# Kernel optimization log

Hardware: AMD Instinct MI355X
Metric: run time of the kernel (lower is better)

The kernel has to match this reference:

```python
import jax, jax.numpy as jnp
import numpy as np

N_HEAD = 16
N_EMBD = 1024
HEAD_DIM = N_EMBD // N_HEAD  # 64
ROPE_BASE = 10000.0


def _rotary_cos_sin(T, dim, dtype=jnp.float32):
    # matches Rotary: inv_freq over even indices, cos/sin cached in bfloat16
    inv_freq = 1.0 / (ROPE_BASE ** (jnp.arange(0, dim, 2, dtype=jnp.float32) / dim))
    freqs = jnp.arange(T, dtype=jnp.float32)[:, None] * inv_freq[None, :]  # [T, dim/2]
    cos = jnp.cos(freqs).astype(jnp.bfloat16).astype(dtype)
    sin = jnp.sin(freqs).astype(jnp.bfloat16).astype(dtype)
    # shape [1, T, 1, dim/2] to broadcast over (B, T, H, d)
    return cos[None, :, None, :], sin[None, :, None, :]


def _apply_rotary(x, cos, sin):
    d = x.shape[3] // 2
    x1, x2 = x[..., :d], x[..., d:]
    y1 = x1 * cos + x2 * sin
    y2 = -x1 * sin + x2 * cos
    return jnp.concatenate([y1, y2], axis=3).astype(x.dtype)


def setup_inputs() -> dict:
    key = jax.random.key(0)
    ks = jax.random.split(key, 8)
    B, T, C = 2, 2048, N_EMBD
    scale = C ** -0.5  # realistic linear-layer init scale
    x = jax.random.normal(ks[0], (B, T, C), dtype=jnp.float32)
    Wq1 = jax.random.normal(ks[1], (C, C), dtype=jnp.float32) * scale
    Wk1 = jax.random.normal(ks[2], (C, C), dtype=jnp.float32) * scale
    Wq2 = jax.random.normal(ks[3], (C, C), dtype=jnp.float32) * scale
    Wk2 = jax.random.normal(ks[4], (C, C), dtype=jnp.float32) * scale
    Wv = jax.random.normal(ks[5], (C, C), dtype=jnp.float32) * scale
    Wout = jax.random.normal(ks[6], (C, C), dtype=jnp.float32) * scale
    return {"x": x, "Wq1": Wq1, "Wk1": Wk1, "Wq2": Wq2, "Wk2": Wk2, "Wv": Wv, "Wout": Wout}


def reference(x, Wq1, Wk1, Wq2, Wk2, Wv, Wout):
    B, T, C = x.shape
    H, D = N_HEAD, HEAD_DIM

    def proj(W):
        # torch nn.Linear(bias=False): y = x @ W.T
        return (x @ W.T).reshape(B, T, H, D)

    q1, k1 = proj(Wq1), proj(Wk1)
    q2, k2 = proj(Wq2), proj(Wk2)
    v = proj(Wv)

    cos, sin = _rotary_cos_sin(T, D, x.dtype)
    q1, k1 = _apply_rotary(q1, cos, sin), _apply_rotary(k1, cos, sin)
    q2, k2 = _apply_rotary(q2, cos, sin), _apply_rotary(k2, cos, sin)

    # two bilinear score maps, elementwise product, causal mask
    s1 = jnp.einsum('bqhd,bkhd->bhqk', q1, k1)  # [B,H,T,T]
    s2 = jnp.einsum('bqhd,bkhd->bhqk', q2, k2)
    causal = jnp.tril(jnp.ones((T, T), dtype=bool))
    pattern = jnp.where(causal[None, None], (s1 / D) * (s2 / D), 0.0)

    y = jnp.einsum('bhqk,bkhd->bqhd', pattern, v).reshape(B, T, C)
    return y @ Wout.T
```

## Files before the change

kernel.cpp:

```cpp
#include <hip/hip_runtime.h>
#include <hip/hip_bf16.h>
#include <math.h>

typedef __bf16 bf16;
typedef __bf16 bf16x8 __attribute__((ext_vector_type(8)));
typedef float  f32x4  __attribute__((ext_vector_type(4)));

#define NB    2
#define NT    2048
#define NH    16
#define ND    64
#define NC    1024
#define NBT   4096
#define NQT   32

#define AS1C(p) ((const __attribute__((address_space(1))) void*)(p))
#define AS3(p)  ((__attribute__((address_space(3))) void*)(p))

#define MFMA(a,b,c) __builtin_amdgcn_mfma_f32_16x16x32_bf16(a, b, c, 0, 0, 0)

struct WPtrs { const float* p[6]; };

__global__ void prep_kernel(const float* __restrict__ x, WPtrs w,
                            bf16* __restrict__ Xbf, bf16* __restrict__ Wcat,
                            float2* __restrict__ tbl)
{
    const int bid = blockIdx.x;
    if (bid < 4096) {
        const int i = (bid * 256 + threadIdx.x) * 4;
        float4 v = *reinterpret_cast<const float4*>(x + i);
        Xbf[i+0] = (bf16)v.x; Xbf[i+1] = (bf16)v.y;
        Xbf[i+2] = (bf16)v.z; Xbf[i+3] = (bf16)v.w;
    } else if (bid < 10240) {
        const int r   = bid - 4096;
        const int mat = r >> 10;
        const int off = ((r & 1023) * 256 + threadIdx.x) * 4;
        float4 v = *reinterpret_cast<const float4*>(w.p[mat] + off);
        bf16* d = Wcat + (size_t)mat * NC * NC + off;
        d[0] = (bf16)v.x; d[1] = (bf16)v.y; d[2] = (bf16)v.z; d[3] = (bf16)v.w;
    } else {
        const int i = (bid - 10240) * 256 + threadIdx.x;
        const int t = i >> 5, j = i & 31;
        float invf = 1.0f / powf(10000.0f, (float)j * (1.0f/32.0f));
        float fr = (float)t * invf;
        float2 cs;
        cs.x = (float)(bf16)cosf(fr);
        cs.y = (float)(bf16)sinf(fr);
        tbl[i] = cs;
    }
}

__global__ __launch_bounds__(256, 3)
void gemm_proj(const bf16* __restrict__ A, const bf16* __restrict__ Bw,
               bf16* __restrict__ qkv, const float2* __restrict__ tbl)
{
    __shared__ bf16 smem[3*8192];

    const int tid  = threadIdx.x;
    const int lane = tid & 63;
    const int w    = tid >> 6;
    const int wr   = w >> 1;
    const int wc   = w & 1;

    const int id  = blockIdx.x;
    const int xcd = id & 7;
    const int r   = id >> 3;
    const int bx  = r >> 2;
    const int by  = xcd * 4 + (r & 3);
    const int row0 = by * 128, col0 = bx * 128;

    const int lo  = lane & 15;
    const int hi  = lane >> 4;

    const int hrow = w*16 + (lane >> 2);
    const int hcol = ((lane & 3) ^ ((lane >> 3) & 3)) * 8;

    f32x4 acc[4][4] = {};

    auto stageHalf = [&](int s, int slot) {
        char* base = (char*)smem + slot * 16384;
        const int k0 = s * 32;
        #pragma unroll
        for (int i = 0; i < 2; ++i) {
            __builtin_amdgcn_global_load_lds(
                AS1C(A + (size_t)(row0 + i*64 + hrow) * NC + k0 + hcol),
                AS3(base + i*4096 + w*1024), 16, 0, 0);
            __builtin_amdgcn_global_load_lds(
                AS1C(Bw + (size_t)(col0 + i*64 + hrow) * NC + k0 + hcol),
                AS3(base + 8192 + i*4096 + w*1024), 16, 0, 0);
        }
    };

    stageHalf(0, 0);
    stageHalf(1, 1);

    const int csw = (lo >> 1) & 3;
    int slot = 0;
    for (int s = 0; s < 32; ++s) {
        if (s < 31) asm volatile("s_waitcnt vmcnt(4)" ::: "memory");
        else        asm volatile("s_waitcnt vmcnt(0)" ::: "memory");
        __builtin_amdgcn_s_barrier();
        asm volatile("" ::: "memory");
        if (s + 2 < 32) {
            int nx = slot + 2; if (nx >= 3) nx -= 3;
            stageHalf(s + 2, nx);
        }

        const char* As = (const char*)smem + slot * 16384;
        const char* Bs = As + 8192;

        bf16x8 af[4], bfr[4];
        #pragma unroll
        for (int m = 0; m < 4; ++m) {
            const int ar = wr*64 + m*16 + lo;
            af[m] = *reinterpret_cast<const bf16x8*>(As + ar*64 + ((hi ^ csw) * 16));
        }
        #pragma unroll
        for (int n = 0; n < 4; ++n) {
            const int br = wc*64 + n*16 + lo;
            bfr[n] = *reinterpret_cast<const bf16x8*>(Bs + br*64 + ((hi ^ csw) * 16));
        }
        __builtin_amdgcn_s_setprio(1);
        #pragma unroll
        for (int m = 0; m < 4; ++m)
            #pragma unroll
            for (int n = 0; n < 4; ++n)
                acc[m][n] = MFMA(af[m], bfr[n], acc[m][n]);
        __builtin_amdgcn_s_setprio(0);

        slot += 1; if (slot >= 3) slot -= 3;
    }
    __syncthreads();

    bf16* Ct = smem;
    const int p  = col0 >> 10;
    const int h0 = (col0 >> 6) & (NH-1);
    const int rb = hi * 4;

    if (p < 4) {
        const float qsc = (p == 0 || p == 2) ? 0.015625f : 1.0f;
        #pragma unroll
        for (int m = 0; m < 4; ++m)
            #pragma unroll
            for (int r2 = 0; r2 < 4; ++r2) {
                const int rl = wr*64 + m*16 + rb + r2;
                const int t  = (row0 + rl) & (NT-1);
                const unsigned key = ((unsigned)(rl >> 2) & 3) << 5;
                #pragma unroll
                for (int n = 0; n < 2; ++n) {
                    const int j = n*16 + lo;
                    float2 cs = tbl[t*32 + j];
                    float a1 = acc[m][n][r2];
                    float a2 = acc[m][n+2][r2];
                    const int c1 = wc*64 + j;
                    const int c2 = c1 + 32;
                    *(bf16*)((char*)Ct + (unsigned)(rl*256 + (((unsigned)c1*2) ^ key)))
                        = (bf16)((a1*cs.x + a2*cs.y) * qsc);
                    *(bf16*)((char*)Ct + (unsigned)(rl*256 + (((unsigned)c2*2) ^ key)))
                        = (bf16)((a2*cs.x - a1*cs.y) * qsc);
                }
            }
        __syncthreads();
        #pragma unroll
        for (int it = 0; it < 8; ++it) {
            const int chunk = it*256 + tid;
            const int rl = chunk >> 4;
            const int cc = chunk & 15;
            const unsigned key = ((unsigned)(rl >> 2) & 3) << 5;
            bf16x8 val = *reinterpret_cast<const bf16x8*>(
                (const char*)Ct + ((unsigned)rl*256 + (((unsigned)cc*16) ^ key)));
            const int rowg = row0 + rl;
            const int b = rowg >> 11;
            const int t = rowg & (NT-1);
            const int hh = h0 + (cc >> 3);
            const int d  = (cc & 7) * 8;
            *reinterpret_cast<bf16x8*>(
                qkv + ((((size_t)p*NB + b)*NH + hh)*NT + t)*ND + d) = val;
        }
    } else {
        #pragma unroll
        for (int m = 0; m < 4; ++m)
            #pragma unroll
            for (int r2 = 0; r2 < 4; ++r2) {
                const int rl = wr*64 + m*16 + rb + r2;
                #pragma unroll
                for (int n = 0; n < 4; ++n) {
                    const int c = wc*64 + n*16 + lo;
                    *(bf16*)((char*)Ct + (unsigned)(c*256 + (((unsigned)rl*2) ^ ((c&7)<<4))))
                        = (bf16)acc[m][n][r2];
                }
            }
        __syncthreads();
        const int b  = row0 >> 11;
        const int t0 = row0 & (NT-1);
        #pragma unroll
        for (int it = 0; it < 8; ++it) {
            const int chunk = it*256 + tid;
            const int c   = chunk >> 4;
            const int tcc = chunk & 15;
            bf16x8 val = *reinterpret_cast<const bf16x8*>(
                (const char*)Ct + (unsigned)(c*256 + (((unsigned)tcc*16) ^ ((c&7)<<4))));
            const int hh = h0 + (c >> 6);
            const int d  = c & 63;
            *reinterpret_cast<bf16x8*>(
                qkv + (((size_t)4*NB + b)*NH + hh)*(size_t)NT*ND
                    + (size_t)d*NT + t0 + tcc*8) = val;
        }
    }
}

__global__ __launch_bounds__(256)
void gemm_out(const bf16* __restrict__ A, const bf16* __restrict__ Bw,
              float* __restrict__ Cp)
{
    __shared__ bf16 smem[4*6144];

    const int tid  = threadIdx.x;
    const int lane = tid & 63;
    const int w    = tid >> 6;
    const int wr   = w >> 1;
    const int wc   = w & 1;
    const int row0 = blockIdx.y * 128;
    const int col0 = blockIdx.x * 64;

    const int lo  = lane & 15;
    const int hi  = lane >> 4;

    const int hrow = w*16 + (lane >> 2);
    const int hcol = ((lane & 3) ^ ((lane >> 3) & 3)) * 8;

    f32x4 acc[4][2] = {};

    auto stageHalf = [&](int s) {
        char* base = (char*)smem + (s & 3) * 12288;
        const int k0 = s * 32;
        #pragma unroll
        for (int i = 0; i < 2; ++i)
            __builtin_amdgcn_global_load_lds(
                AS1C(A + (size_t)(row0 + i*64 + hrow) * NC + k0 + hcol),
                AS3(base + i*4096 + w*1024), 16, 0, 0);
        __builtin_amdgcn_global_load_lds(
            AS1C(Bw + (size_t)(col0 + hrow) * NC + k0 + hcol),
            AS3(base + 8192 + w*1024), 16, 0, 0);
    };

    stageHalf(0);
    stageHalf(1);

    const int csw = (lo >> 1) & 3;
    for (int s = 0; s < 32; ++s) {
        if (s < 31) asm volatile("s_waitcnt vmcnt(3)" ::: "memory");
        else        asm volatile("s_waitcnt vmcnt(0)" ::: "memory");
        __builtin_amdgcn_s_barrier();
        asm volatile("" ::: "memory");
        if (s + 2 < 32) stageHalf(s + 2);

        const char* As = (const char*)smem + (s & 3) * 12288;
        const char* Bs = As + 8192;

        bf16x8 af[4], bfr[2];
        #pragma unroll
        for (int m = 0; m < 4; ++m) {
            const int ar = wr*64 + m*16 + lo;
            af[m] = *reinterpret_cast<const bf16x8*>(As + ar*64 + ((hi ^ csw) * 16));
        }
        #pragma unroll
        for (int n = 0; n < 2; ++n) {
            const int br = wc*32 + n*16 + lo;
            bfr[n] = *reinterpret_cast<const bf16x8*>(Bs + br*64 + ((hi ^ csw) * 16));
        }
        __builtin_amdgcn_s_setprio(1);
        #pragma unroll
        for (int m = 0; m < 4; ++m)
            #pragma unroll
            for (int n = 0; n < 2; ++n)
                acc[m][n] = MFMA(af[m], bfr[n], acc[m][n]);
        __builtin_amdgcn_s_setprio(0);
    }

    const int rb = hi * 4;
    #pragma unroll
    for (int m = 0; m < 4; ++m)
        #pragma unroll
        for (int n = 0; n < 2; ++n)
            #pragma unroll
            for (int r = 0; r < 4; ++r) {
                int row = row0 + wr*64 + m*16 + rb + r;
                int col = col0 + wc*32 + n*16 + lo;
                Cp[(size_t)row * NC + col] = acc[m][n][r];
            }
}

__global__ __launch_bounds__(256, 2)
void attn_kernel(const bf16* __restrict__ qkv, bf16* __restrict__ Y)
{
    __shared__ bf16 K1s[3*4096];
    __shared__ bf16 K2s[3*4096];
    __shared__ bf16 Vts[3*4096];
    __shared__ bf16 Pl [4][1024];

    const int tid  = threadIdx.x;
    const int lane = tid & 63;
    const int w    = tid >> 6;

    const int lin  = blockIdx.x;
    const int xcd  = lin & 7;
    const int slot = lin >> 3;
    const int pair = xcd * 4 + (slot >> 4);
    const int qa   = slot & 15;
    const int h    = pair >> 1;
    const int b    = pair & 1;
    const int qb   = NQT - 1 - qa;

    const size_t plane = (size_t)NB * NH * NT * ND;
    const size_t bh    = ((size_t)b * NH + h) * (size_t)NT * ND;
    const bf16* Q1 = qkv + 0*plane + bh;
    const bf16* K1 = qkv + 1*plane + bh;
    const bf16* Q2 = qkv + 2*plane + bh;
    const bf16* K2 = qkv + 3*plane + bh;
    const bf16* V  = qkv + 4*plane + bh;

    const int lo  = lane & 15;
    const int hi  = lane >> 4;
    const int hi8 = hi * 8;

    bf16x8 q1fa[2], q2fa[2], q1fb[2], q2fb[2];
    #pragma unroll
    for (int dd = 0; dd < 2; ++dd) {
        const size_t ra  = (size_t)(qa*64 + w*16 + lo) * ND + dd*32 + hi8;
        const size_t rbq = (size_t)(qb*64 + w*16 + lo) * ND + dd*32 + hi8;
        q1fa[dd] = *reinterpret_cast<const bf16x8*>(Q1 + ra);
        q2fa[dd] = *reinterpret_cast<const bf16x8*>(Q2 + ra);
        q1fb[dd] = *reinterpret_cast<const bf16x8*>(Q1 + rbq);
        q2fb[dd] = *reinterpret_cast<const bf16x8*>(Q2 + rbq);
    }

    f32x4 yacca[4] = {}, yaccb[4] = {};

    const int srow = tid >> 3;
    const int ssw  = ((tid & 7) ^ (srow & 7)) * 8;

    auto stageK = [&](int buf, int k0) {
        #pragma unroll
        for (int i = 0; i < 2; ++i) {
            const unsigned loff = (unsigned)(buf*8192 + i*4096 + w*1024);
            __builtin_amdgcn_global_load_lds(
                AS1C(K1 + (size_t)(k0 + i*32 + srow) * ND + ssw),
                AS3((char*)K1s + loff), 16, 0, 0);
            __builtin_amdgcn_global_load_lds(
                AS1C(K2 + (size_t)(k0 + i*32 + srow) * ND + ssw),
                AS3((char*)K2s + loff), 16, 0, 0);
        }
    };
    auto stageVT = [&](int buf, int k0) {
        #pragma unroll
        for (int i = 0; i < 2; ++i) {
            const int inst = w*2 + i;
            const int d    = inst*8 + (lane >> 3);
            const int sc   = ((lane & 7) ^ ((lane >> 3) & 7)) * 8;
            __builtin_amdgcn_global_load_lds(
                AS1C(V + (size_t)d * NT + k0 + sc),
                AS3((char*)Vts + (unsigned)(buf*8192 + inst*1024)), 16, 0, 0);
        }
    };

    stageK(0, 0);  stageVT(0, 0);
    stageK(1, 64); stageVT(1, 64);

    int cur = 0;
    for (int kt = 0; kt <= qb; ++kt) {
        if (kt < qb) asm volatile("s_waitcnt vmcnt(6)" ::: "memory");
        else         asm volatile("s_waitcnt vmcnt(0)" ::: "memory");
        __builtin_amdgcn_s_barrier();
        asm volatile("" ::: "memory");
        if (kt + 2 <= qb) {
            int nx = cur + 2; if (nx >= 3) nx -= 3;
            stageK(nx, (kt + 2) * 64);
            stageVT(nx, (kt + 2) * 64);
        }

        const bool doA = (kt <= qa);
        const bf16* K1b = K1s + cur*4096;
        const bf16* K2b = K2s + cur*4096;
        const char* Vb  = (const char*)Vts + cur*8192;

        f32x4 s1a[4] = {}, s2a[4] = {}, s1b[4] = {}, s2b[4] = {};
        __builtin_amdgcn_s_setprio(1);
        #pragma unroll
        for (int dd = 0; dd < 2; ++dd)
            #pragma unroll
            for (int sub = 0; sub < 4; ++sub) {
                const unsigned kb = (unsigned)((sub*16 + lo)*128 + (((dd*4 + hi) ^ (lo & 7)) * 16));
                bf16x8 k1f = *reinterpret_cast<const bf16x8*>((const char*)K1b + kb);
                bf16x8 k2f = *reinterpret_cast<const bf16x8*>((const char*)K2b + kb);
                s1b[sub] = MFMA(q1fb[dd], k1f, s1b[sub]);
                s2b[sub] = MFMA(q2fb[dd], k2f, s2b[sub]);
                if (doA) {
                    s1a[sub] = MFMA(q1fa[dd], k1f, s1a[sub]);
                    s2a[sub] = MFMA(q2fa[dd], k2f, s2a[sub]);
                }
            }
        __builtin_amdgcn_s_setprio(0);

        #define COMBINE(S1, S2, DIAG)                                                  \
            _Pragma("unroll")                                                          \
            for (int sub = 0; sub < 4; ++sub)                                          \
                _Pragma("unroll")                                                      \
                for (int r = 0; r < 4; ++r) {                                          \
                    const int row = hi*4 + r;                                          \
                    const int col = sub*16 + lo;                                       \
                    const unsigned byte = (unsigned)(row*128 + (((col>>3) ^ (row&7))*16) + (col&7)*2); \
                    float pv = S1[sub][r] * S2[sub][r];                                \
                    if (DIAG && col > w*16 + row) pv = 0.0f;                           \
                    *(bf16*)((char*)Pl[w] + byte) = (bf16)pv;                          \
                }

        if (kt == qb) { COMBINE(s1b, s2b, true) } else { COMBINE(s1b, s2b, false) }
        asm volatile("s_waitcnt lgkmcnt(0)" ::: "memory");
        __builtin_amdgcn_sched_barrier(0);

        bf16x8 vfr[2][4];
        __builtin_amdgcn_s_setprio(1);
        #pragma unroll
        for (int ks = 0; ks < 2; ++ks) {
            const unsigned pby = (unsigned)(lo*128 + (((ks*4 + hi) ^ (lo & 7)) * 16));
            bf16x8 pfb = *reinterpret_cast<const bf16x8*>((const char*)Pl[w] + pby);
            #pragma unroll
            for (int n = 0; n < 4; ++n) {
                const unsigned vby = (unsigned)((n*16 + lo)*128 + (((ks*4 + hi) ^ (lo & 7)) * 16));
                vfr[ks][n] = *reinterpret_cast<const bf16x8*>(Vb + vby);
                yaccb[n] = MFMA(pfb, vfr[ks][n], yaccb[n]);
            }
        }
        __builtin_amdgcn_s_setprio(0);

        if (doA) {
            asm volatile("s_waitcnt lgkmcnt(0)" ::: "memory");
            __builtin_amdgcn_sched_barrier(0);
            if (kt == qa) { COMBINE(s1a, s2a, true) } else { COMBINE(s1a, s2a, false) }
            asm volatile("s_waitcnt lgkmcnt(0)" ::: "memory");
            __builtin_amdgcn_sched_barrier(0);
            __builtin_amdgcn_s_setprio(1);
            #pragma unroll
            for (int ks = 0; ks < 2; ++ks) {
                const unsigned pby = (unsigned)(lo*128 + (((ks*4 + hi) ^ (lo & 7)) * 16));
                bf16x8 pfa = *reinterpret_cast<const bf16x8*>((const char*)Pl[w] + pby);
                #pragma unroll
                for (int n = 0; n < 4; ++n)
                    yacca[n] = MFMA(pfa, vfr[ks][n], yacca[n]);
            }
            __builtin_amdgcn_s_setprio(0);
        }
        #undef COMBINE

        cur += 1; if (cur >= 3) cur -= 3;
    }

    auto writeOut = [&](int q0, const f32x4* ya) {
        #pragma unroll
        for (int n = 0; n < 4; ++n)
            #pragma unroll
            for (int r = 0; r < 4; ++r) {
                const int row = hi*4 + r;
                const int col = n*16 + lo;
                const unsigned byte = (unsigned)(row*128 + (((col>>3) ^ (row&7))*16) + (col&7)*2);
                *(bf16*)((char*)Pl[w] + byte) = (bf16)ya[n][r];
            }
        asm volatile("s_waitcnt lgkmcnt(0)" ::: "memory");
        __builtin_amdgcn_sched_barrier(0);
        #pragma unroll
        for (int pass = 0; pass < 2; ++pass) {
            const int idx = pass*64 + lane;
            const int row = idx >> 3;
            const int cc  = idx & 7;
            bf16x8 val = *reinterpret_cast<const bf16x8*>(
                (const char*)Pl[w] + row*128 + ((cc ^ (row&7))*16));
            const int t = q0 + w*16 + row;
            const int c = h*ND + cc*8;
            *reinterpret_cast<bf16x8*>(Y + ((size_t)b*NT + t)*NC + c) = val;
        }
    };
    writeOut(qa*64, yacca);
    writeOut(qb*64, yaccb);
}

extern "C" void kernel_launch(void* const* d_in, const int* in_sizes, int n_in,
                              void* d_out, int out_size, void* d_ws, size_t ws_size,
                              hipStream_t stream)
{
    const float* x = (const float*)d_in[0];

    char* ws = (char*)d_ws;
    bf16*   Xbf   = (bf16*)ws;
    bf16*   Wcat  = (bf16*)(ws + (size_t)NBT*NC*2);
    bf16*   QKV   = (bf16*)(ws + (size_t)NBT*NC*2 + (size_t)6*NC*NC*2);
    bf16*   Ybf   = (bf16*)((char*)QKV + (size_t)5*NBT*NC*2);
    float2* tbl   = (float2*)((char*)Ybf + (size_t)NBT*NC*2);
    bf16*   Woutb = Wcat + (size_t)5*NC*NC;

    WPtrs wp;
    wp.p[0] = (const float*)d_in[1]; wp.p[1] = (const float*)d_in[2];
    wp.p[2] = (const float*)d_in[3]; wp.p[3] = (const float*)d_in[4];
    wp.p[4] = (const float*)d_in[5]; wp.p[5] = (const float*)d_in[6];

    prep_kernel<<<dim3(10496), 256, 0, stream>>>(x, wp, Xbf, Wcat, tbl);

    gemm_proj<<<dim3(1280), 256, 0, stream>>>(Xbf, Wcat, QKV, tbl);
    attn_kernel<<<dim3(512), 256, 0, stream>>>(QKV, Ybf);
    gemm_out<<<dim3(NC/64, NBT/128), 256, 0, stream>>>(Ybf, Woutb, (float*)d_out);
}
```

Baseline: 137.6 us.

## Split paired query tiles across 8 waves with 128-key double-buffered chunks

The attention kernel moves from 4 waves that each handle both paired query tiles (qa and qb) to 8 waves per block, with waves 0-3 taking tile qb and waves 4-7 taking qa. K/V staging changes from a 3-deep ring of 64-key tiles to a 2-deep double buffer of 128-key chunks, waiting for all loads with vmcnt(0) each iteration. Each wave now computes 16x128 score blocks and drops the V-fragment register sharing between the two tiles. This is meant to add parallelism and shorten the serial per-wave loop. In exchange it costs more LDS per block, gives up the deeper prefetch, and leaves the qa waves idle for later chunks, which may cause imbalance.

```diff
diff --git a/kernel.cpp b/kernel.cpp
--- a/kernel.cpp
+++ b/kernel.cpp
@@ -291,17 +291,19 @@
             }
 }
 
-__global__ __launch_bounds__(256, 2)
+__global__ __launch_bounds__(512, 2)
 void attn_kernel(const bf16* __restrict__ qkv, bf16* __restrict__ Y)
 {
-    __shared__ bf16 K1s[3*4096];
-    __shared__ bf16 K2s[3*4096];
-    __shared__ bf16 Vts[3*4096];
-    __shared__ bf16 Pl [4][1024];
+    __shared__ bf16 K1s[2][128*64];
+    __shared__ bf16 K2s[2][128*64];
+    __shared__ bf16 Vts[2][64*128];
+    __shared__ bf16 Pl [8][16*128];
 
     const int tid  = threadIdx.x;
     const int lane = tid & 63;
     const int w    = tid >> 6;
+    const int ta   = w >> 2;
+    const int w4   = w & 3;
 
     const int lin  = blockIdx.x;
     const int xcd  = lin & 7;
@@ -311,6 +313,7 @@
     const int h    = pair >> 1;
     const int b    = pair & 1;
     const int qb   = NQT - 1 - qa;
+    const int qw   = ta ? qa : qb;
 
     const size_t plane = (size_t)NB * NH * NT * ND;
     const size_t bh    = ((size_t)b * NH + h) * (size_t)NT * ND;
@@ -323,165 +326,124 @@
     const int lo  = lane & 15;
     const int hi  = lane >> 4;
     const int hi8 = hi * 8;
-
-    bf16x8 q1fa[2], q2fa[2], q1fb[2], q2fb[2];
+    const int qg0 = qw*64 + w4*16;
+
+    bf16x8 q1f[2], q2f[2];
     #pragma unroll
     for (int dd = 0; dd < 2; ++dd) {
-        const size_t ra  = (size_t)(qa*64 + w*16 + lo) * ND + dd*32 + hi8;
-        const size_t rbq = (size_t)(qb*64 + w*16 + lo) * ND + dd*32 + hi8;
-        q1fa[dd] = *reinterpret_cast<const bf16x8*>(Q1 + ra);
-        q2fa[dd] = *reinterpret_cast<const bf16x8*>(Q2 + ra);
-        q1fb[dd] = *reinterpret_cast<const bf16x8*>(Q1 + rbq);
-        q2fb[dd] = *reinterpret_cast<const bf16x8*>(Q2 + rbq);
-    }
-
-    f32x4 yacca[4] = {}, yaccb[4] = {};
+        const size_t ra = (size_t)(qg0 + lo) * ND + dd*32 + hi8;
+        q1f[dd] = *reinterpret_cast<const bf16x8*>(Q1 + ra);
+        q2f[dd] = *reinterpret_cast<const bf16x8*>(Q2 + ra);
+    }
+
+    f32x4 yacc[4] = {};
 
     const int srow = tid >> 3;
     const int ssw  = ((tid & 7) ^ (srow & 7)) * 8;
-
-    auto stageK = [&](int buf, int k0) {
-        #pragma unroll
-        for (int i = 0; i < 2; ++i) {
-            const unsigned loff = (unsigned)(buf*8192 + i*4096 + w*1024);
-            __builtin_amdgcn_global_load_lds(
-                AS1C(K1 + (size_t)(k0 + i*32 + srow) * ND + ssw),
-                AS3((char*)K1s + loff), 16, 0, 0);
-            __builtin_amdgcn_global_load_lds(
-                AS1C(K2 + (size_t)(k0 + i*32 + srow) * ND + ssw),
-                AS3((char*)K2s + loff), 16, 0, 0);
+    const int vdl = tid >> 4;
+    const int vsc = ((tid & 15) ^ (vdl & 15)) * 8;
+
+    auto stage = [&](int buf, int k0) {
+        #pragma unroll
+        for (int j = 0; j < 2; ++j) {
+            const unsigned loff = (unsigned)(j*8192 + w*1024);
+            __builtin_amdgcn_global_load_lds(
+                AS1C(K1 + (size_t)(k0 + j*64 + srow) * ND + ssw),
+                AS3((char*)K1s[buf] + loff), 16, 0, 0);
+            __builtin_amdgcn_global_load_lds(
+                AS1C(K2 + (size_t)(k0 + j*64 + srow) * ND + ssw),
+                AS3((char*)K2s[buf] + loff), 16, 0, 0);
+            __builtin_amdgcn_global_load_lds(
+                AS1C(V + (size_t)(j*32 + vdl) * NT + k0 + vsc),
+                AS3((char*)Vts[buf] + loff), 16, 0, 0);
         }
     };
-    auto stageVT = [&](int buf, int k0) {
-        #pragma unroll
-        for (int i = 0; i < 2; ++i) {
-            const int inst = w*2 + i;
-            const int d    = inst*8 + (lane >> 3);
-            const int sc   = ((lane & 7) ^ ((lane >> 3) & 7)) * 8;
-            __builtin_amdgcn_global_load_lds(
-                AS1C(V + (size_t)d * NT + k0 + sc),
-                AS3((char*)Vts + (unsigned)(buf*8192 + inst*1024)), 16, 0, 0);
-        }
-    };
-
-    stageK(0, 0);  stageVT(0, 0);
-    stageK(1, 64); stageVT(1, 64);
+
+    const int nck = (qb >> 1) + 1;
+    const int mya = qw >> 1;
+
+    stage(0, 0);
 
     int cur = 0;
-    for (int kt = 0; kt <= qb; ++kt) {
-        if (kt < qb) asm volatile("s_waitcnt vmcnt(6)" ::: "memory");
-        else         asm volatile("s_waitcnt vmcnt(0)" ::: "memory");
+    for (int ckt = 0; ckt < nck; ++ckt) {
+        asm volatile("s_waitcnt vmcnt(0)" ::: "memory");
         __builtin_amdgcn_s_barrier();
         asm volatile("" ::: "memory");
-        if (kt + 2 <= qb) {
-            int nx = cur + 2; if (nx >= 3) nx -= 3;
-            stageK(nx, (kt + 2) * 64);
-            stageVT(nx, (kt + 2) * 64);
-        }
-
-        const bool doA = (kt <= qa);
-        const bf16* K1b = K1s + cur*4096;
-        const bf16* K2b = K2s + cur*4096;
-        const char* Vb  = (const char*)Vts + cur*8192;
-
-        f32x4 s1a[4] = {}, s2a[4] = {}, s1b[4] = {}, s2b[4] = {};
-        __builtin_amdgcn_s_setprio(1);
-        #pragma unroll
-        for (int dd = 0; dd < 2; ++dd)
-            #pragma unroll
-            for (int sub = 0; sub < 4; ++sub) {
-                const unsigned kb = (unsigned)((sub*16 + lo)*128 + (((dd*4 + hi) ^ (lo & 7)) * 16));
-                bf16x8 k1f = *reinterpret_cast<const bf16x8*>((const char*)K1b + kb);
-                bf16x8 k2f = *reinterpret_cast<const bf16x8*>((const char*)K2b + kb);
-                s1b[sub] = MFMA(q1fb[dd], k1f, s1b[sub]);
-                s2b[sub] = MFMA(q2fb[dd], k2f, s2b[sub]);
-                if (doA) {
-                    s1a[sub] = MFMA(q1fa[dd], k1f, s1a[sub]);
-                    s2a[sub] = MFMA(q2fa[dd], k2f, s2a[sub]);
+        if (ckt + 1 < nck) stage(cur ^ 1, (ckt + 1) * 128);
+
+        if (ckt <= mya) {
+            const char* K1b = (const char*)K1s[cur];
+            const char* K2b = (const char*)K2s[cur];
+
+            f32x4 s1[8] = {}, s2[8] = {};
+            __builtin_amdgcn_s_setprio(1);
+            #pragma unroll
+            for (int dd = 0; dd < 2; ++dd)
+                #pragma unroll
+                for (int sub = 0; sub < 8; ++sub) {
+                    const unsigned kb = (unsigned)((sub*16 + lo)*128 + (((dd*4 + hi) ^ (lo & 7)) * 16));
+                    bf16x8 k1f = *reinterpret_cast<const bf16x8*>(K1b + kb);
+                    bf16x8 k2f = *reinterpret_cast<const bf16x8*>(K2b + kb);
+                    s1[sub] = MFMA(q1f[dd], k1f, s1[sub]);
+                    s2[sub] = MFMA(q2f[dd], k2f, s2[sub]);
+                }
+            __builtin_amdgcn_s_setprio(0);
+
+            const bool diag = (ckt == mya);
+            #pragma unroll
+            for (int sub = 0; sub < 8; ++sub)
+                #pragma unroll
+                for (int r = 0; r < 4; ++r) {
+                    const int row = hi*4 + r;
+                    const int col = sub*16 + lo;
+                    const unsigned byte = (unsigned)(row*256 + (((col>>3) ^ (row&15))*16) + (col&7)*2);
+                    float pv = s1[sub][r] * s2[sub][r];
+                    if (diag && (ckt*128 + col > qg0 + row)) pv = 0.0f;
+                    *(bf16*)((char*)Pl[w] + byte) = (bf16)pv;
+                }
+            asm volatile("s_waitcnt lgkmcnt(0)" ::: "memory");
+            __builtin_amdgcn_sched_barrier(0);
+
+            const char* Vb = (const char*)Vts[cur];
+            __builtin_amdgcn_s_setprio(1);
+            #pragma unroll
+            for (int ks = 0; ks < 4; ++ks) {
+                const unsigned pby = (unsigned)(lo*256 + (((ks*4 + hi) ^ lo) * 16));
+                bf16x8 pf = *reinterpret_cast<const bf16x8*>((const char*)Pl[w] + pby);
+                #pragma unroll
+                for (int n = 0; n < 4; ++n) {
+                    const unsigned vby = (unsigned)((n*16 + lo)*256 + (((ks*4 + hi) ^ lo) * 16));
+                    bf16x8 vf = *reinterpret_cast<const bf16x8*>(Vb + vby);
+                    yacc[n] = MFMA(pf, vf, yacc[n]);
                 }
             }
-        __builtin_amdgcn_s_setprio(0);
-
-        #define COMBINE(S1, S2, DIAG)                                                  \
-            _Pragma("unroll")                                                          \
-            for (int sub = 0; sub < 4; ++sub)                                          \
-                _Pragma("unroll")                                                      \
-                for (int r = 0; r < 4; ++r) {                                          \
-                    const int row = hi*4 + r;                                          \
-                    const int col = sub*16 + lo;                                       \
-                    const unsigned byte = (unsigned)(row*128 + (((col>>3) ^ (row&7))*16) + (col&7)*2); \
-                    float pv = S1[sub][r] * S2[sub][r];                                \
-                    if (DIAG && col > w*16 + row) pv = 0.0f;                           \
-                    *(bf16*)((char*)Pl[w] + byte) = (bf16)pv;                          \
-                }
-
-        if (kt == qb) { COMBINE(s1b, s2b, true) } else { COMBINE(s1b, s2b, false) }
-        asm volatile("s_waitcnt lgkmcnt(0)" ::: "memory");
-        __builtin_amdgcn_sched_barrier(0);
-
-        bf16x8 vfr[2][4];
-        __builtin_amdgcn_s_setprio(1);
-        #pragma unroll
-        for (int ks = 0; ks < 2; ++ks) {
-            const unsigned pby = (unsigned)(lo*128 + (((ks*4 + hi) ^ (lo & 7)) * 16));
-            bf16x8 pfb = *reinterpret_cast<const bf16x8*>((const char*)Pl[w] + pby);
-            #pragma unroll
-            for (int n = 0; n < 4; ++n) {
-                const unsigned vby = (unsigned)((n*16 + lo)*128 + (((ks*4 + hi) ^ (lo & 7)) * 16));
-                vfr[ks][n] = *reinterpret_cast<const bf16x8*>(Vb + vby);
-                yaccb[n] = MFMA(pfb, vfr[ks][n], yaccb[n]);
-            }
-        }
-        __builtin_amdgcn_s_setprio(0);
-
-        if (doA) {
-            asm volatile("s_waitcnt lgkmcnt(0)" ::: "memory");
-            __builtin_amdgcn_sched_barrier(0);
-            if (kt == qa) { COMBINE(s1a, s2a, true) } else { COMBINE(s1a, s2a, false) }
-            asm volatile("s_waitcnt lgkmcnt(0)" ::: "memory");
-            __builtin_amdgcn_sched_barrier(0);
-            __builtin_amdgcn_s_setprio(1);
-            #pragma unroll
-            for (int ks = 0; ks < 2; ++ks) {
-                const unsigned pby = (unsigned)(lo*128 + (((ks*4 + hi) ^ (lo & 7)) * 16));
-                bf16x8 pfa = *reinterpret_cast<const bf16x8*>((const char*)Pl[w] + pby);
-                #pragma unroll
-                for (int n = 0; n < 4; ++n)
-                    yacca[n] = MFMA(pfa, vfr[ks][n], yacca[n]);
-            }
             __builtin_amdgcn_s_setprio(0);
         }
-        #undef COMBINE
-
-        cur += 1; if (cur >= 3) cur -= 3;
-    }
-
-    auto writeOut = [&](int q0, const f32x4* ya) {
-        #pragma unroll
-        for (int n = 0; n < 4; ++n)
-            #pragma unroll
-            for (int r = 0; r < 4; ++r) {
-                const int row = hi*4 + r;
-                const int col = n*16 + lo;
-                const unsigned byte = (unsigned)(row*128 + (((col>>3) ^ (row&7))*16) + (col&7)*2);
-                *(bf16*)((char*)Pl[w] + byte) = (bf16)ya[n][r];
-            }
-        asm volatile("s_waitcnt lgkmcnt(0)" ::: "memory");
-        __builtin_amdgcn_sched_barrier(0);
-        #pragma unroll
-        for (int pass = 0; pass < 2; ++pass) {
-            const int idx = pass*64 + lane;
-            const int row = idx >> 3;
-            const int cc  = idx & 7;
-            bf16x8 val = *reinterpret_cast<const bf16x8*>(
-                (const char*)Pl[w] + row*128 + ((cc ^ (row&7))*16));
-            const int t = q0 + w*16 + row;
-            const int c = h*ND + cc*8;
-            *reinterpret_cast<bf16x8*>(Y + ((size_t)b*NT + t)*NC + c) = val;
-        }
-    };
-    writeOut(qa*64, yacca);
-    writeOut(qb*64, yaccb);
+        cur ^= 1;
+    }
+
+    #pragma unroll
+    for (int n = 0; n < 4; ++n)
+        #pragma unroll
+        for (int r = 0; r < 4; ++r) {
+            const int row = hi*4 + r;
+            const int col = n*16 + lo;
+            const unsigned byte = (unsigned)(row*256 + (((col>>3) ^ (row&7))*16) + (col&7)*2);
+            *(bf16*)((char*)Pl[w] + byte) = (bf16)yacc[n][r];
+        }
+    asm volatile("s_waitcnt lgkmcnt(0)" ::: "memory");
+    __builtin_amdgcn_sched_barrier(0);
+    #pragma unroll
+    for (int pass = 0; pass < 2; ++pass) {
+        const int idx = pass*64 + lane;
+        const int row = idx >> 3;
+        const int cc  = idx & 7;
+        bf16x8 val = *reinterpret_cast<const bf16x8*>(
+            (const char*)Pl[w] + row*256 + ((cc ^ (row&7))*16));
+        const int t = qg0 + row;
+        const int c = h*ND + cc*8;
+        *reinterpret_cast<bf16x8*>(Y + ((size_t)b*NT + t)*NC + c) = val;
+    }
 }
 
 extern "C" void kernel_launch(void* const* d_in, const int* in_sizes, int n_in,
@@ -506,6 +468,6 @@
     prep_kernel<<<dim3(10496), 256, 0, stream>>>(x, wp, Xbf, Wcat, tbl);
 
     gemm_proj<<<dim3(1280), 256, 0, stream>>>(Xbf, Wcat, QKV, tbl);
-    attn_kernel<<<dim3(512), 256, 0, stream>>>(QKV, Ybf);
+    attn_kernel<<<dim3(512), 512, 0, stream>>>(QKV, Ybf);
     gemm_out<<<dim3(NC/64, NBT/128), 256, 0, stream>>>(Ybf, Woutb, (float*)d_out);
 }
```

Result: slower. 150.2 us (+9.1%).
